# Optimization experiments

Measured on AMD Instinct MI355X. Metric: run time of the kernel, lower is better.

The kernel has to match this reference:

```python
import jax, jax.numpy as jnp
import numpy as np

N_NODES = 100000
N_EDGES = 1600000
IN_DIM, HID, OUT_DIM = 128, 128, 64


def _glorot(key, fan_in, fan_out):
    s = float(np.sqrt(6.0 / (fan_in + fan_out)))
    return jax.random.uniform(key, (fan_in, fan_out), jnp.float32, -s, s)


def setup_inputs() -> dict:
    key = jax.random.key(0)
    ks = jax.random.split(key, 6)
    x = jax.random.normal(ks[0], (N_NODES, IN_DIM), jnp.float32)
    edge_index = jax.random.randint(ks[1], (2, N_EDGES), 0, N_NODES, jnp.int32)
    return {
        "x": x,
        "edge_index": edge_index,
        "W0": _glorot(ks[2], IN_DIM, HID), "b0": jnp.zeros((HID,), jnp.float32),
        "W1": _glorot(ks[3], HID, HID),    "b1": jnp.zeros((HID,), jnp.float32),
        "W2": _glorot(ks[4], HID, OUT_DIM), "b2": jnp.zeros((OUT_DIM,), jnp.float32),
    }


def _gcn_conv(x, src, dst, norm, W, b):
    # x' = D^{-1/2} (A+I) D^{-1/2} X W + b  (PyG GCNConv, add_self_loops=True)
    h = x @ W                       # [N, F_out]
    msg = h[src] * norm[:, None]    # [E+N, F_out] gathered, normalized messages
    out = jax.ops.segment_sum(msg, dst, num_segments=x.shape[0])
    return out + b


def reference(x, edge_index, W0, b0, W1, b1, W2, b2):
    n = x.shape[0]
    loop = jnp.arange(n, dtype=edge_index.dtype)
    src = jnp.concatenate([edge_index[0], loop])  # self-loops appended
    dst = jnp.concatenate([edge_index[1], loop])
    deg = jax.ops.segment_sum(jnp.ones_like(src, jnp.float32), dst, num_segments=n)
    dis = jnp.where(deg > 0, jax.lax.rsqrt(jnp.maximum(deg, 1e-12)), 0.0)
    norm = dis[src] * dis[dst]      # symmetric GCN normalization per edge

    h = jax.nn.relu(_gcn_conv(x, src, dst, norm, W0, b0))
    h = jax.nn.relu(_gcn_conv(h, src, dst, norm, W1, b1))
    h = jax.nn.relu(_gcn_conv(h, src, dst, norm, W2, b2))
    return jax.nn.log_softmax(h, axis=1)
```

## Files before the change

### kernel.cpp

```cpp
#include <hip/hip_runtime.h>

#define NN 100000
#define NE 1600000
#define NBK 782
#define NBLK 256
#define CHUNK ((NE + NBLK - 1) / NBLK)

typedef __bf16 bf16x4 __attribute__((ext_vector_type(4)));
typedef __bf16 bf16x8 __attribute__((ext_vector_type(8)));
typedef float f32x2 __attribute__((ext_vector_type(2)));
typedef float f32x4 __attribute__((ext_vector_type(4)));

#define ACC8_FP8(vv)                                                                  \
  {                                                                                   \
    f32x2 p;                                                                          \
    p = __builtin_amdgcn_cvt_pk_f32_fp8((vv).x, 0); acc[0] += p[0]; acc[1] += p[1];   \
    p = __builtin_amdgcn_cvt_pk_f32_fp8((vv).x, 1); acc[2] += p[0]; acc[3] += p[1];   \
    p = __builtin_amdgcn_cvt_pk_f32_fp8((vv).y, 0); acc[4] += p[0]; acc[5] += p[1];   \
    p = __builtin_amdgcn_cvt_pk_f32_fp8((vv).y, 1); acc[6] += p[0]; acc[7] += p[1];   \
  }


__global__ __launch_bounds__(256) void kW_prep(const float* __restrict__ W0, const float* __restrict__ W1,
                                               const float* __restrict__ W2, __bf16* __restrict__ Wt) {
  int i = blockIdx.x * 256 + threadIdx.x;
  if (i < 16384) {
    int k = i >> 7, n = i & 127;
    Wt[n * 128 + k] = (__bf16)W0[i];
  } else if (i < 32768) {
    int j = i - 16384;
    int k = j >> 7, n = j & 127;
    Wt[16384 + n * 128 + k] = (__bf16)W1[j];
  } else if (i < 40960) {
    int j = i - 32768;
    int k = j >> 6, n = j & 63;
    Wt[32768 + n * 128 + k] = (__bf16)W2[j];
  }
}


__global__ __launch_bounds__(256) void k1_hist(const int* __restrict__ dst, int* __restrict__ bhist) {
  __shared__ int h[NBK];
  int tid = threadIdx.x, b = blockIdx.x;
  for (int i = tid; i < NBK; i += 256) h[i] = 0;
  __syncthreads();
  int base = b * CHUNK, end = min(base + CHUNK, NE);
  for (int e = base + tid; e < end; e += 256) atomicAdd(&h[dst[e] >> 7], 1);
  __syncthreads();
  for (int i = tid; i < NBK; i += 256) bhist[i * NBLK + b] = h[i];
}

__global__ __launch_bounds__(256) void kA2(const int* __restrict__ bhist, int* __restrict__ btot) {
  int w = threadIdx.x >> 6, lane = threadIdx.x & 63;
  int bin = blockIdx.x * 4 + w;
  if (bin >= NBK) return;
  int4 v = *(const int4*)(bhist + bin * NBLK + lane * 4);
  int s = v.x + v.y + v.z + v.w;
#pragma unroll
  for (int off = 32; off > 0; off >>= 1) s += __shfl_xor(s, off);
  if (lane == 0) btot[bin] = s;
}

__global__ __launch_bounds__(1024) void kB_bscan(const int* __restrict__ btot, int* __restrict__ bptr) {
  __shared__ int s[1024];
  int tid = threadIdx.x;
  int v = (tid < NBK) ? btot[tid] : 0;
  s[tid] = v;
  __syncthreads();
  for (int off = 1; off < 1024; off <<= 1) {
    int t = (tid >= off) ? s[tid - off] : 0;
    __syncthreads();
    s[tid] += t;
    __syncthreads();
  }
  if (tid < NBK) bptr[tid + 1] = s[tid];
  if (tid == 0) bptr[0] = 0;
}

__global__ __launch_bounds__(256) void kC2(const int* __restrict__ bhist, const int* __restrict__ bptr,
                                           int* __restrict__ blockbase) {
  int w = threadIdx.x >> 6, lane = threadIdx.x & 63;
  int bin = blockIdx.x * 4 + w;
  if (bin >= NBK) return;
  int4 v = *(const int4*)(bhist + bin * NBLK + lane * 4);
  int ls = v.x + v.y + v.z + v.w;
  int incl = ls;
#pragma unroll
  for (int off = 1; off < 64; off <<= 1) {
    int t = __shfl_up(incl, off);
    if (lane >= off) incl += t;
  }
  int base = bptr[bin] + incl - ls;
  int4 o;
  o.x = base;
  o.y = base + v.x;
  o.z = base + v.x + v.y;
  o.w = base + v.x + v.y + v.z;
  *(int4*)(blockbase + bin * NBLK + lane * 4) = o;
}

__global__ __launch_bounds__(256) void k3_scatter(const int* __restrict__ src, const int* __restrict__ dst,
                                                  const int* __restrict__ blockbase, int* __restrict__ bucketed) {
  __shared__ int cur[NBK];
  int tid = threadIdx.x, b = blockIdx.x;
  for (int i = tid; i < NBK; i += 256) cur[i] = blockbase[i * NBLK + b];
  __syncthreads();
  int base = b * CHUNK, end = min(base + CHUNK, NE);
  for (int e = base + tid; e < end; e += 256) {
    int d = dst[e];
    int pos = atomicAdd(&cur[d >> 7], 1);
    bucketed[pos] = (src[e] << 7) | (d & 127);
  }
}

__global__ __launch_bounds__(256) void k_degfill(const int* __restrict__ bucketed, const int* __restrict__ bptr,
                                                 int* __restrict__ row_ptr, float* __restrict__ dis,
                                                 int* __restrict__ csr_src) {
  __shared__ int deg[128];
  __shared__ int sc[128];
  __shared__ int cur[128];
  int b = blockIdx.x, tid = threadIdx.x;
  int nb0 = b << 7;
  if (tid < 128) deg[tid] = 0;
  __syncthreads();
  int beg = bptr[b], end = bptr[b + 1];
  for (int e = beg + tid; e < end; e += 256) atomicAdd(&deg[bucketed[e] & 127], 1);
  __syncthreads();
  if (tid < 128) sc[tid] = deg[tid];
  __syncthreads();
  for (int off = 1; off < 128; off <<= 1) {
    int t = (tid >= off && tid < 128) ? sc[tid - off] : 0;
    __syncthreads();
    if (tid < 128) sc[tid] += t;
    __syncthreads();
  }
  if (tid < 128) {
    cur[tid] = beg + sc[tid] - deg[tid];
    if (nb0 + tid < NN) {
      row_ptr[nb0 + tid + 1] = beg + sc[tid];
      dis[nb0 + tid] = rsqrtf((float)(deg[tid] + 1));
      if (b == 0 && tid == 0) row_ptr[0] = 0;
    }
  }
  __syncthreads();
  for (int e = beg + tid; e < end; e += 256) {
    int pk = bucketed[e];
    int pos = atomicAdd(&cur[pk & 127], 1);
    csr_src[pos] = pk >> 7;
  }
}


template <int BN, int MODE, bool OUT8>
__global__ __launch_bounds__(256) void k_gemm(const void* __restrict__ Av, const __bf16* __restrict__ Wt,
                                              const float* __restrict__ bias, const float* __restrict__ dis,
                                              void* __restrict__ outv) {
  constexpr int LDK = 136;
  constexpr int NT = BN / 32;
  constexpr int ROWB = BN * (OUT8 ? 1 : 2);
  __shared__ __bf16 lB[BN * LDK];

  const int tid = threadIdx.x;
  const int rowBase = blockIdx.x * 128;
  const int lane = tid & 63;
  const int wid = tid >> 6;
  const int wm = (wid & 1) * 64;
  const int wn = (wid >> 1) * (BN / 2);
  const int lm = lane & 15;
  const int kg = lane >> 4;

  if (blockIdx.x == 0 && tid < ROWB / 16) {
    ((uint4*)((char*)outv + (size_t)NN * ROWB))[tid] = make_uint4(0, 0, 0, 0);
  }

  for (int c = tid; c < 16 * BN; c += 256) {
    int n = c >> 4;
    int koff = (c & 15) * 8;
    bf16x8 w = *(const bf16x8*)(Wt + n * 128 + koff);
    *(bf16x8*)&lB[n * LDK + koff] = w;
  }
  __syncthreads();

  f32x4 acc[4][NT] = {};
  const bool full = (rowBase + 128 <= NN);

#pragma unroll 2
  for (int ks = 0; ks < 128; ks += 32) {
    int k0 = ks + kg * 8;
    bf16x8 af[4];
    if constexpr (MODE == 0) {
      const float* A = (const float*)Av;
#pragma unroll
      for (int tm = 0; tm < 4; ++tm) {
        int gr = rowBase + wm + tm * 16 + lm;
        f32x4 a0 = {}, a1 = {};
        if (full || gr < NN) {
          a0 = *(const f32x4*)(A + (size_t)gr * 128 + k0);
          a1 = *(const f32x4*)(A + (size_t)gr * 128 + k0 + 4);
        }
        af[tm] = bf16x8{(__bf16)a0[0], (__bf16)a0[1], (__bf16)a0[2], (__bf16)a0[3],
                        (__bf16)a1[0], (__bf16)a1[1], (__bf16)a1[2], (__bf16)a1[3]};
      }
    } else {
      const __bf16* A = (const __bf16*)Av;
      f32x4 b0 = *(const f32x4*)(bias + k0);
      f32x4 b1 = *(const f32x4*)(bias + k0 + 4);
#pragma unroll
      for (int tm = 0; tm < 4; ++tm) {
        int gr = rowBase + wm + tm * 16 + lm;
        bf16x8 v = {};
        if (full || gr < NN) v = *(const bf16x8*)(A + (size_t)gr * 128 + k0);
        af[tm] = bf16x8{(__bf16)fmaxf((float)v[0] + b0[0], 0.f), (__bf16)fmaxf((float)v[1] + b0[1], 0.f),
                        (__bf16)fmaxf((float)v[2] + b0[2], 0.f), (__bf16)fmaxf((float)v[3] + b0[3], 0.f),
                        (__bf16)fmaxf((float)v[4] + b1[0], 0.f), (__bf16)fmaxf((float)v[5] + b1[1], 0.f),
                        (__bf16)fmaxf((float)v[6] + b1[2], 0.f), (__bf16)fmaxf((float)v[7] + b1[3], 0.f)};
      }
    }
    bf16x8 bfr[NT];
#pragma unroll
    for (int tn = 0; tn < NT; ++tn)
      bfr[tn] = *(const bf16x8*)&lB[(wn + tn * 16 + lm) * LDK + k0];
#pragma unroll
    for (int tm = 0; tm < 4; ++tm)
#pragma unroll
      for (int tn = 0; tn < NT; ++tn)
        acc[tm][tn] = __builtin_amdgcn_mfma_f32_16x16x32_bf16(af[tm], bfr[tn], acc[tm][tn], 0, 0, 0);
  }

#pragma unroll
  for (int tm = 0; tm < 4; ++tm) {
    int r0 = rowBase + wm + tm * 16 + kg * 4;
#pragma unroll
    for (int tn = 0; tn < NT; ++tn) {
      int c0 = wn + tn * 16 + lm;
#pragma unroll
      for (int r = 0; r < 4; ++r) {
        int gr = r0 + r;
        if (full || gr < NN) {
          float val = acc[tm][tn][r] * dis[gr];
          if constexpr (OUT8) {
            unsigned char* o8 = (unsigned char*)outv;
            unsigned pk = __builtin_amdgcn_cvt_pk_fp8_f32(val, val, 0, 0);
            o8[(size_t)gr * BN + c0] = (unsigned char)(pk & 0xffu);
          } else {
            __bf16* ob = (__bf16*)outv;
            ob[(size_t)gr * BN + c0] = (__bf16)val;
          }
        }
      }
    }
  }
}


__global__ __launch_bounds__(256) void k_agg128(const unsigned char* __restrict__ tmp8, const int* __restrict__ row_ptr,
                                                const int* __restrict__ csr_src, const float* __restrict__ dis,
                                                __bf16* __restrict__ agg) {
  int wid = (blockIdx.x * 256 + threadIdx.x) >> 6;
  int lane = threadIdx.x & 63;
  if (wid >= NN) return;
  int grp = lane >> 4;
  int fl = lane & 15;

  int beg = row_ptr[wid];
  int end = row_ptr[wid + 1];

  float acc[8] = {0.f, 0.f, 0.f, 0.f, 0.f, 0.f, 0.f, 0.f};
  if (grp == 0) {
    uint2 sv = *(const uint2*)(tmp8 + (size_t)wid * 128 + fl * 8);
    ACC8_FP8(sv);
  }

  for (int base = beg; base < end; base += 64) {
    int cnt = min(64, end - base);
    int sidx = (base + lane < end) ? csr_src[base + lane] : NN;
    int i = 0;
    while (i < cnt) {
      int rem = cnt - i;
      if (rem > 16) {
        uint2 v[8];
#pragma unroll
        for (int u = 0; u < 8; ++u) {
          int s = __shfl(sidx, (i + u * 4 + grp) & 63);
          v[u] = *(const uint2*)(tmp8 + (size_t)s * 128 + fl * 8);
        }
#pragma unroll
        for (int u = 0; u < 8; ++u) ACC8_FP8(v[u]);
        i += 32;
      } else {
        uint2 v[4];
#pragma unroll
        for (int u = 0; u < 4; ++u) {
          int s = __shfl(sidx, (i + u * 4 + grp) & 63);
          v[u] = *(const uint2*)(tmp8 + (size_t)s * 128 + fl * 8);
        }
#pragma unroll
        for (int u = 0; u < 4; ++u) ACC8_FP8(v[u]);
        i += 16;
      }
    }
  }

#pragma unroll
  for (int t = 0; t < 8; ++t) acc[t] += __shfl_xor(acc[t], 16);
#pragma unroll
  for (int t = 0; t < 8; ++t) acc[t] += __shfl_xor(acc[t], 32);

  if (grp == 0) {
    float d = dis[wid];
    bf16x8 o;
#pragma unroll
    for (int t = 0; t < 8; ++t) o[t] = (__bf16)(acc[t] * d);
    *(bf16x8*)&agg[(size_t)wid * 128 + fl * 8] = o;
  }
}


__global__ __launch_bounds__(256) void k_agg64_final(const __bf16* __restrict__ tmp, const int* __restrict__ row_ptr,
                                                     const int* __restrict__ csr_src, const float* __restrict__ dis,
                                                     const float* __restrict__ b2, float* __restrict__ out) {
  int wid = (blockIdx.x * 256 + threadIdx.x) >> 6;
  int lane = threadIdx.x & 63;
  int grp = lane >> 4;
  int fl = lane & 15;

  int beg = row_ptr[wid];
  int end = row_ptr[wid + 1];

  float acc[4] = {0.f, 0.f, 0.f, 0.f};
  if (grp == 0) {
    bf16x4 sv = *(const bf16x4*)&tmp[(size_t)wid * 64 + fl * 4];
#pragma unroll
    for (int t = 0; t < 4; ++t) acc[t] = (float)sv[t];
  }

  for (int base = beg; base < end; base += 64) {
    int cnt = min(64, end - base);
    int sidx = (base + lane < end) ? csr_src[base + lane] : NN;
    int i = 0;
    while (i < cnt) {
      int rem = cnt - i;
      if (rem > 16) {
        bf16x4 v[8];
#pragma unroll
        for (int u = 0; u < 8; ++u) {
          int s = __shfl(sidx, (i + u * 4 + grp) & 63);
          v[u] = *(const bf16x4*)&tmp[(size_t)s * 64 + fl * 4];
        }
#pragma unroll
        for (int u = 0; u < 8; ++u)
#pragma unroll
          for (int t = 0; t < 4; ++t) acc[t] += (float)v[u][t];
        i += 32;
      } else {
        bf16x4 v[4];
#pragma unroll
        for (int u = 0; u < 4; ++u) {
          int s = __shfl(sidx, (i + u * 4 + grp) & 63);
          v[u] = *(const bf16x4*)&tmp[(size_t)s * 64 + fl * 4];
        }
#pragma unroll
        for (int u = 0; u < 4; ++u)
#pragma unroll
          for (int t = 0; t < 4; ++t) acc[t] += (float)v[u][t];
        i += 16;
      }
    }
  }

#pragma unroll
  for (int t = 0; t < 4; ++t) acc[t] += __shfl_xor(acc[t], 16);
#pragma unroll
  for (int t = 0; t < 4; ++t) acc[t] += __shfl_xor(acc[t], 32);

  float d = dis[wid];
  float v[4], lm = -1e30f;
#pragma unroll
  for (int t = 0; t < 4; ++t) {
    v[t] = fmaxf(acc[t] * d + b2[fl * 4 + t], 0.f);
    lm = fmaxf(lm, v[t]);
  }
#pragma unroll
  for (int off = 8; off > 0; off >>= 1) lm = fmaxf(lm, __shfl_xor(lm, off));
  float le = 0.f;
#pragma unroll
  for (int t = 0; t < 4; ++t) le += __expf(v[t] - lm);
#pragma unroll
  for (int off = 8; off > 0; off >>= 1) le += __shfl_xor(le, off);
  float ls = lm + __logf(le);
  if (grp == 0) {
    f32x4 o = {v[0] - ls, v[1] - ls, v[2] - ls, v[3] - ls};
    *(f32x4*)&out[(size_t)wid * 64 + fl * 4] = o;
  }
}


extern "C" void kernel_launch(void* const* d_in, const int* in_sizes, int n_in,
                              void* d_out, int out_size, void* d_ws, size_t ws_size,
                              hipStream_t stream) {
  const float* x  = (const float*)d_in[0];
  const int*   ei = (const int*)d_in[1];
  const float* W0 = (const float*)d_in[2];
  const float* b0 = (const float*)d_in[3];
  const float* W1 = (const float*)d_in[4];
  const float* b1 = (const float*)d_in[5];
  const float* W2 = (const float*)d_in[6];
  const float* b2 = (const float*)d_in[7];
  const int* esrc = ei;
  const int* edst = ei + NE;

  char* p = (char*)d_ws;
  auto alloc = [&](size_t bytes) {
    char* q = p;
    p += (bytes + 255) & ~(size_t)255;
    return q;
  };
  float*  dis     = (float*)alloc((size_t)NN * 4);
  int*    row_ptr = (int*)alloc((size_t)(NN + 1) * 4);
  int*    btot    = (int*)alloc(NBK * 4);
  int*    bptr    = (int*)alloc((NBK + 1) * 4);
  __bf16* Wt      = (__bf16*)alloc(40960 * 2);
  int*    csr_src = (int*)alloc((size_t)NE * 4);
  char*   tmp     = (char*)alloc((size_t)(NN + 1) * 128 * 2);
  unsigned char* tmp8 = (unsigned char*)tmp;
  __bf16* tmp16   = (__bf16*)tmp;
  int*    bucketed  = (int*)tmp;
  int*    bhist     = csr_src;
  int*    blockbase = csr_src + NBLK * NBK;

  kW_prep<<<160, 256, 0, stream>>>(W0, W1, W2, Wt);
  k1_hist<<<NBLK, 256, 0, stream>>>(edst, bhist);
  kA2<<<(NBK + 3) / 4, 256, 0, stream>>>(bhist, btot);
  kB_bscan<<<1, 1024, 0, stream>>>(btot, bptr);
  kC2<<<(NBK + 3) / 4, 256, 0, stream>>>(bhist, bptr, blockbase);
  k3_scatter<<<NBLK, 256, 0, stream>>>(esrc, edst, blockbase, bucketed);
  k_degfill<<<NBK, 256, 0, stream>>>(bucketed, bptr, row_ptr, dis, csr_src);

  int gblocks = (NN + 127) / 128;
  int ablocks = (NN * 64 + 255) / 256;

  k_gemm<128, 0, true><<<gblocks, 256, 0, stream>>>(x, Wt, nullptr, dis, tmp8);
  k_agg128<<<ablocks, 256, 0, stream>>>(tmp8, row_ptr, csr_src, dis, (__bf16*)d_out);

  k_gemm<128, 2, true><<<gblocks, 256, 0, stream>>>(d_out, Wt + 16384, b0, dis, tmp8);
  k_agg128<<<ablocks, 256, 0, stream>>>(tmp8, row_ptr, csr_src, dis, (__bf16*)d_out);

  k_gemm<64, 2, false><<<gblocks, 256, 0, stream>>>(d_out, Wt + 32768, b1, dis, tmp16);
  k_agg64_final<<<ablocks, 256, 0, stream>>>(tmp16, row_ptr, csr_src, dis, b2, (float*)d_out);
}
```

Before: 364.0 us.

## Merge weight prep into histogram kernel, warp-scan block totals, prefetch GEMM A tiles

Weight transposition and conversion now runs inside extra blocks of the histogram kernel, which removes one kernel launch. The block-total scan switches from a 10-step shared-memory Hillis-Steele loop to wave shuffles plus a small cross-wave scan. The GEMM loads every A fragment for all four k-steps into registers before staging the weights into LDS, so global latency overlaps the LDS fill. The prefetch raises register pressure, most of all in the fp32 MODE 0 path with 32 f32x4 values per thread, and may lower occupancy.

```diff
diff --git a/kernel.cpp b/kernel.cpp
--- a/kernel.cpp
+++ b/kernel.cpp
@@ -21,27 +21,28 @@
   }
 
 
-__global__ __launch_bounds__(256) void kW_prep(const float* __restrict__ W0, const float* __restrict__ W1,
+__global__ __launch_bounds__(256) void k1_hist(const int* __restrict__ dst, int* __restrict__ bhist,
+                                               const float* __restrict__ W0, const float* __restrict__ W1,
                                                const float* __restrict__ W2, __bf16* __restrict__ Wt) {
-  int i = blockIdx.x * 256 + threadIdx.x;
-  if (i < 16384) {
-    int k = i >> 7, n = i & 127;
-    Wt[n * 128 + k] = (__bf16)W0[i];
-  } else if (i < 32768) {
-    int j = i - 16384;
-    int k = j >> 7, n = j & 127;
-    Wt[16384 + n * 128 + k] = (__bf16)W1[j];
-  } else if (i < 40960) {
-    int j = i - 32768;
-    int k = j >> 6, n = j & 63;
-    Wt[32768 + n * 128 + k] = (__bf16)W2[j];
-  }
-}
-
-
-__global__ __launch_bounds__(256) void k1_hist(const int* __restrict__ dst, int* __restrict__ bhist) {
+  int b = blockIdx.x;
+  if (b >= NBLK) {
+    int i = (b - NBLK) * 256 + threadIdx.x;
+    if (i < 16384) {
+      int k = i >> 7, n = i & 127;
+      Wt[n * 128 + k] = (__bf16)W0[i];
+    } else if (i < 32768) {
+      int j = i - 16384;
+      int k = j >> 7, n = j & 127;
+      Wt[16384 + n * 128 + k] = (__bf16)W1[j];
+    } else if (i < 40960) {
+      int j = i - 32768;
+      int k = j >> 6, n = j & 63;
+      Wt[32768 + n * 128 + k] = (__bf16)W2[j];
+    }
+    return;
+  }
   __shared__ int h[NBK];
-  int tid = threadIdx.x, b = blockIdx.x;
+  int tid = threadIdx.x;
   for (int i = tid; i < NBK; i += 256) h[i] = 0;
   __syncthreads();
   int base = b * CHUNK, end = min(base + CHUNK, NE);
@@ -62,18 +63,29 @@
 }
 
 __global__ __launch_bounds__(1024) void kB_bscan(const int* __restrict__ btot, int* __restrict__ bptr) {
-  __shared__ int s[1024];
-  int tid = threadIdx.x;
+  __shared__ int ws[16];
+  int tid = threadIdx.x, lane = tid & 63, w = tid >> 6;
   int v = (tid < NBK) ? btot[tid] : 0;
-  s[tid] = v;
-  __syncthreads();
-  for (int off = 1; off < 1024; off <<= 1) {
-    int t = (tid >= off) ? s[tid - off] : 0;
-    __syncthreads();
-    s[tid] += t;
-    __syncthreads();
-  }
-  if (tid < NBK) bptr[tid + 1] = s[tid];
+  int incl = v;
+#pragma unroll
+  for (int off = 1; off < 64; off <<= 1) {
+    int t = __shfl_up(incl, off);
+    if (lane >= off) incl += t;
+  }
+  if (lane == 63) ws[w] = incl;
+  __syncthreads();
+  if (tid < 16) {
+    int s = ws[tid];
+    int si = s;
+#pragma unroll
+    for (int off = 1; off < 16; off <<= 1) {
+      int t = __shfl_up(si, off);
+      if (lane >= off) si += t;
+    }
+    ws[tid] = si - s;
+  }
+  __syncthreads();
+  if (tid < NBK) bptr[tid + 1] = incl + ws[w];
   if (tid == 0) bptr[0] = 0;
 }
 
@@ -168,9 +180,34 @@
   const int wn = (wid >> 1) * (BN / 2);
   const int lm = lane & 15;
   const int kg = lane >> 4;
+  const bool full = (rowBase + 128 <= NN);
 
   if (blockIdx.x == 0 && tid < ROWB / 16) {
     ((uint4*)((char*)outv + (size_t)NN * ROWB))[tid] = make_uint4(0, 0, 0, 0);
+  }
+
+  f32x4 a0[4][4], a1[4][4];
+  bf16x8 araw[4][4];
+#pragma unroll
+  for (int ks4 = 0; ks4 < 4; ++ks4) {
+    int k0 = ks4 * 32 + kg * 8;
+#pragma unroll
+    for (int tm = 0; tm < 4; ++tm) {
+      int gr = rowBase + wm + tm * 16 + lm;
+      if constexpr (MODE == 0) {
+        const float* A = (const float*)Av;
+        a0[ks4][tm] = f32x4{};
+        a1[ks4][tm] = f32x4{};
+        if (full || gr < NN) {
+          a0[ks4][tm] = *(const f32x4*)(A + (size_t)gr * 128 + k0);
+          a1[ks4][tm] = *(const f32x4*)(A + (size_t)gr * 128 + k0 + 4);
+        }
+      } else {
+        const __bf16* A = (const __bf16*)Av;
+        araw[ks4][tm] = bf16x8{};
+        if (full || gr < NN) araw[ks4][tm] = *(const bf16x8*)(A + (size_t)gr * 128 + k0);
+      }
+    }
   }
 
   for (int c = tid; c < 16 * BN; c += 256) {
@@ -182,34 +219,24 @@
   __syncthreads();
 
   f32x4 acc[4][NT] = {};
-  const bool full = (rowBase + 128 <= NN);
-
-#pragma unroll 2
-  for (int ks = 0; ks < 128; ks += 32) {
-    int k0 = ks + kg * 8;
+
+#pragma unroll
+  for (int ks4 = 0; ks4 < 4; ++ks4) {
+    int k0 = ks4 * 32 + kg * 8;
     bf16x8 af[4];
     if constexpr (MODE == 0) {
-      const float* A = (const float*)Av;
 #pragma unroll
       for (int tm = 0; tm < 4; ++tm) {
-        int gr = rowBase + wm + tm * 16 + lm;
-        f32x4 a0 = {}, a1 = {};
-        if (full || gr < NN) {
-          a0 = *(const f32x4*)(A + (size_t)gr * 128 + k0);
-          a1 = *(const f32x4*)(A + (size_t)gr * 128 + k0 + 4);
-        }
-        af[tm] = bf16x8{(__bf16)a0[0], (__bf16)a0[1], (__bf16)a0[2], (__bf16)a0[3],
-                        (__bf16)a1[0], (__bf16)a1[1], (__bf16)a1[2], (__bf16)a1[3]};
+        f32x4 A0 = a0[ks4][tm], A1 = a1[ks4][tm];
+        af[tm] = bf16x8{(__bf16)A0[0], (__bf16)A0[1], (__bf16)A0[2], (__bf16)A0[3],
+                        (__bf16)A1[0], (__bf16)A1[1], (__bf16)A1[2], (__bf16)A1[3]};
       }
     } else {
-      const __bf16* A = (const __bf16*)Av;
       f32x4 b0 = *(const f32x4*)(bias + k0);
       f32x4 b1 = *(const f32x4*)(bias + k0 + 4);
 #pragma unroll
       for (int tm = 0; tm < 4; ++tm) {
-        int gr = rowBase + wm + tm * 16 + lm;
-        bf16x8 v = {};
-        if (full || gr < NN) v = *(const bf16x8*)(A + (size_t)gr * 128 + k0);
+        bf16x8 v = araw[ks4][tm];
         af[tm] = bf16x8{(__bf16)fmaxf((float)v[0] + b0[0], 0.f), (__bf16)fmaxf((float)v[1] + b0[1], 0.f),
                         (__bf16)fmaxf((float)v[2] + b0[2], 0.f), (__bf16)fmaxf((float)v[3] + b0[3], 0.f),
                         (__bf16)fmaxf((float)v[4] + b1[0], 0.f), (__bf16)fmaxf((float)v[5] + b1[1], 0.f),
@@ -428,8 +455,7 @@
   int*    bhist     = csr_src;
   int*    blockbase = csr_src + NBLK * NBK;
 
-  kW_prep<<<160, 256, 0, stream>>>(W0, W1, W2, Wt);
-  k1_hist<<<NBLK, 256, 0, stream>>>(edst, bhist);
+  k1_hist<<<NBLK + 160, 256, 0, stream>>>(edst, bhist, W0, W1, W2, Wt);
   kA2<<<(NBK + 3) / 4, 256, 0, stream>>>(bhist, btot);
   kB_bscan<<<1, 1024, 0, stream>>>(btot, bptr);
   kC2<<<(NBK + 3) / 4, 256, 0, stream>>>(bhist, bptr, blockbase);
```

New measurement: 376.3 us. 1.03x slower.
